# Kernel tuning notes

Hardware: AMD Instinct MI355X
Metric: run time of the kernel (lower is better)

The kernel has to match this reference:

```python
import jax, jax.numpy as jnp
import numpy as np

K = 20  # hard-coded in LPDNet


def act(v):
    # LeakyReLU with negative_slope=0.0 == ReLU
    return jnp.maximum(v, 0.0)


def conv1d(x, w, b):
    # x: (B,C,N), w: (O,C), b: (O,) -> (B,O,N)  (1x1 Conv1d)
    return jnp.einsum('bcn,oc->bon', x, w) + b[None, :, None]


def conv2d(x, w, b):
    # x: (B,C,N,K), w: (O,C), b: (O,) -> (B,O,N,K)  (1x1 Conv2d)
    return jnp.einsum('bcnk,oc->bonk', x, w) + b[None, :, None, None]


def knn(x, k):
    # x: (B,C,N) -> idx (B,N,k) of nearest neighbors by negative squared L2
    xx = jnp.sum(x * x, axis=1)                       # (B,N)
    inner = jnp.einsum('bcn,bcm->bnm', x, x)          # (B,N,N)
    pairwise = 2.0 * inner - xx[:, :, None] - xx[:, None, :]
    _, idx = jax.lax.top_k(pairwise, k)
    return idx


def graph_feature(x, idx):
    # x: (B,C,N), idx: (B,N,k) -> (B,2C,N,k) as concat(neighbor - center, center)
    xt = jnp.transpose(x, (0, 2, 1))                  # (B,N,C)
    nbr = jax.vmap(lambda f, i: f[i])(xt, idx)        # (B,N,k,C)
    ctr = jnp.broadcast_to(xt[:, :, None, :], nbr.shape)
    feat = jnp.concatenate([nbr - ctr, ctr], axis=-1)  # (B,N,k,2C)
    return jnp.transpose(feat, (0, 3, 1, 2))          # (B,2C,N,k)


def setup_inputs():
    key = jax.random.key(0)
    ks = jax.random.split(key, 13)
    p = lambda k, s: jax.random.normal(k, s, jnp.float32) * 0.02
    return {
        'x': jax.random.normal(ks[0], (8, 1, 4096, 3), jnp.float32),
        'w1': p(ks[1], (64, 3)),    'b1': p(ks[2], (64,)),
        'w2': p(ks[3], (64, 64)),   'b2': p(ks[4], (64,)),
        'wdg1': p(ks[5], (128, 128)), 'bdg1': p(ks[6], (128,)),
        'wdg2': p(ks[7], (128, 128)), 'bdg2': p(ks[8], (128,)),
        'wsn1': p(ks[9], (256, 256)), 'bsn1': p(ks[10], (256,)),
        'w3': p(ks[11], (1024, 512)), 'b3': p(ks[12], (1024,)),
    }


def reference(x, w1, b1, w2, b2, wdg1, bdg1, wdg2, bdg2, wsn1, bsn1, w3, b3):
    xp = jnp.transpose(jnp.squeeze(x, 1), (0, 2, 1))  # (B,3,N)
    xinit = xp
    h = act(conv1d(xp, w1, b1))                       # (B,64,N)
    h = act(conv1d(h, w2, b2))                        # (B,64,N)
    idx1 = knn(h, K)
    g = graph_feature(h, idx1)                        # (B,128,N,K)
    g = act(conv2d(g, wdg1, bdg1))                    # (B,128,N,K)
    x1 = jnp.max(g, axis=-1)                          # (B,128,N)
    g = act(conv2d(g, wdg2, bdg2))                    # (B,128,N,K)
    x2 = jnp.max(g, axis=-1)                          # (B,128,N)
    idx2 = knn(xinit, K)                              # knn on raw 3D coords
    g = graph_feature(x2, idx2)                       # (B,256,N,K)
    g = act(conv2d(g, wsn1, bsn1))                    # (B,256,N,K)
    x3 = jnp.max(g, axis=-1)                          # (B,256,N)
    cat = jnp.concatenate([x1, x2, x3], axis=1)       # (B,512,N)
    out = act(conv1d(cat, w3, b3))                    # (B,1024,N)
    return out[..., None]                             # (B,1024,N,1)
```

## Files before the change

kernel.cpp:

```cpp
#include <hip/hip_runtime.h>
#include <stdint.h>


#define NB 8
#define NP 4096
#define NPTS (NB*NP)

typedef float  floatx4 __attribute__((ext_vector_type(4)));
typedef short  short8  __attribute__((ext_vector_type(8)));

__device__ __forceinline__ unsigned short f2bf(float f) {
  union { float f; uint32_t u; } v; v.f = f;
  uint32_t r = v.u + 0x7fffu + ((v.u >> 16) & 1u);
  return (unsigned short)(r >> 16);
}
__device__ __forceinline__ float bf2f(unsigned short h) {
  union { uint32_t u; float f; } v; v.u = ((uint32_t)h) << 16;
  return v.f;
}

__device__ __forceinline__ floatx4 mfma_bf16(short8 a, short8 b, floatx4 c) {
  return __builtin_amdgcn_mfma_f32_16x16x32_bf16(a, b, c, 0, 0, 0);
}

__global__ void cvt_weights(const float* wdg1, unsigned short* wdg1b,
                            const float* wdg2, unsigned short* wdg2b,
                            const float* wsn1, unsigned short* wsn1b,
                            const float* w3, unsigned short* w3b) {
  int i = blockIdx.x * 256 + threadIdx.x;
  if (i < 16384) {
    int c = i & 127;
    wdg1b[i] = f2bf(wdg1[i] - (c >= 64 ? wdg1[i - 64] : 0.f));
  }
  if (i < 16384) wdg2b[i] = f2bf(wdg2[i]);
  if (i < 65536) {
    int c = i & 255;
    wsn1b[i] = f2bf(wsn1[i] - (c >= 128 ? wsn1[i - 128] : 0.f));
  }
  if (i < 524288) w3b[i] = f2bf(w3[i]);
}

__global__ __launch_bounds__(256) void conv12(
    const float* __restrict__ xin, const float* __restrict__ w1,
    const float* __restrict__ b1, const float* __restrict__ w2,
    const float* __restrict__ b2,
    unsigned short* __restrict__ hb16, unsigned short* __restrict__ hlo16,
    float* __restrict__ hh, float* __restrict__ cc) {
  int wave = threadIdx.x >> 6, lane = threadIdx.x & 63;
  int p = blockIdx.x * 4 + wave;
  __shared__ float s_h1[4][64];
  const float* xp = xin + p * 3;
  float c0 = xp[0], c1 = xp[1], c2 = xp[2];
  float v = b1[lane] + w1[lane*3+0]*c0 + w1[lane*3+1]*c1 + w1[lane*3+2]*c2;
  s_h1[wave][lane] = fmaxf(v, 0.f);
  __syncthreads();
  float acc = b2[lane];
  const float* wr = w2 + lane * 64;
  #pragma unroll
  for (int c = 0; c < 64; c += 4) {
    floatx4 w4 = *(const floatx4*)(wr + c);
    acc += w4[0]*s_h1[wave][c]   + w4[1]*s_h1[wave][c+1]
         + w4[2]*s_h1[wave][c+2] + w4[3]*s_h1[wave][c+3];
  }
  acc = fmaxf(acc, 0.f);
  unsigned short hi = f2bf(acc);
  hb16[p*64 + lane] = hi;
  hlo16[p*64 + lane] = f2bf(acc - bf2f(hi));
  float sq = acc * acc;
  #pragma unroll
  for (int off = 32; off; off >>= 1) sq += __shfl_xor(sq, off, 64);
  if (lane == 0) { hh[p] = sq; cc[p] = c0*c0 + c1*c1 + c2*c2; }
}

__global__ __launch_bounds__(256) void knn64_mfma(
    const unsigned short* __restrict__ Hhi, const unsigned short* __restrict__ Hlo,
    const float* __restrict__ XX, int* __restrict__ idx_out) {
  __shared__ unsigned short mhi[128][72];
  __shared__ unsigned short mlo[128][72];
  __shared__ float dots[64][132];
  __shared__ float xxMh[128];
  __shared__ float tau[64];
  int b = blockIdx.y;
  int r0 = blockIdx.x * 64;
  int t = threadIdx.x;
  int lane = t & 63, wave = t >> 6;
  int quad = lane >> 4, l15 = lane & 15;
  const unsigned short* Hhib = Hhi + (size_t)b * NP * 64;
  const unsigned short* Hlob = Hlo + (size_t)b * NP * 64;
  short8 ahi[2], alo[2];
  {
    const unsigned short* pr = Hhib + (size_t)(r0 + wave * 16 + l15) * 64 + quad * 8;
    const unsigned short* pl = Hlob + (size_t)(r0 + wave * 16 + l15) * 64 + quad * 8;
    ahi[0] = *(const short8*)pr; ahi[1] = *(const short8*)(pr + 32);
    alo[0] = *(const short8*)pl; alo[1] = *(const short8*)(pl + 32);
  }
  if (t < 64) tau[t] = -__builtin_inff();

  float lv[20]; int li[20];
  #pragma unroll
  for (int s = 0; s < 20; s++) { lv[s] = -__builtin_inff(); li[s] = 0x7fffffff; }
  float minval = -__builtin_inff(); int minpos = 0;
  int row = t >> 2, sub = t & 3;

  for (int mt = 0; mt < NP / 128; mt++) {
    int m0 = mt * 128;
    {
      int hf = t & 1, r = (t >> 1) & 127;
      int c0 = hf * 32;
      const unsigned short* sh = Hhib + (size_t)(m0 + r) * 64 + c0;
      const unsigned short* sl = Hlob + (size_t)(m0 + r) * 64 + c0;
      *(short8*)&mhi[r][c0]      = *(const short8*)sh;
      *(short8*)&mhi[r][c0 + 8]  = *(const short8*)(sh + 8);
      *(short8*)&mhi[r][c0 + 16] = *(const short8*)(sh + 16);
      *(short8*)&mhi[r][c0 + 24] = *(const short8*)(sh + 24);
      *(short8*)&mlo[r][c0]      = *(const short8*)sl;
      *(short8*)&mlo[r][c0 + 8]  = *(const short8*)(sl + 8);
      *(short8*)&mlo[r][c0 + 16] = *(const short8*)(sl + 16);
      *(short8*)&mlo[r][c0 + 24] = *(const short8*)(sl + 24);
    }
    if (t < 128) xxMh[t] = 0.5f * XX[b * NP + m0 + t];
    __syncthreads();
    #pragma unroll
    for (int nt = 0; nt < 8; nt++) {
      floatx4 acc = (floatx4)0.f;
      #pragma unroll
      for (int ks = 0; ks < 2; ks++) {
        int k0 = ks * 32 + quad * 8;
        short8 bhi = *(short8*)&mhi[nt * 16 + l15][k0];
        short8 blo = *(short8*)&mlo[nt * 16 + l15][k0];
        acc = mfma_bf16(ahi[ks], bhi, acc);
        acc = mfma_bf16(ahi[ks], blo, acc);
        acc = mfma_bf16(alo[ks], bhi, acc);
        acc = mfma_bf16(alo[ks], blo, acc);
      }
      int colg = nt * 16 + l15;
      float xm = xxMh[colg];
      #pragma unroll
      for (int r = 0; r < 4; r++) {
        int mr = wave * 16 + quad * 4 + r;
        dots[mr][colg] = acc[r] - xm;
      }
    }
    __syncthreads();
    float gate = fmaxf(minval, tau[row]);
    floatx4 dv[8];
    #pragma unroll
    for (int q = 0; q < 8; q++) dv[q] = *(floatx4*)&dots[row][sub * 32 + q * 4];
    uint32_t mask = 0;
    #pragma unroll
    for (int q = 0; q < 8; q++)
      #pragma unroll
      for (int j = 0; j < 4; j++)
        if (dv[q][j] > gate) mask |= 1u << (q * 4 + j);
    #pragma clang loop unroll(disable)
    for (int round = 0; round < 32; round++) {
      if (!__any(mask != 0)) break;
      if (mask) {
        int i = __builtin_ctz(mask); mask &= mask - 1;
        float v = dots[row][sub * 32 + i];
        if (v > minval) {
          int gi = m0 + sub * 32 + i;
          #pragma unroll
          for (int s = 0; s < 20; s++)
            if (s == minpos) { lv[s] = v; li[s] = gi; }
          minval = __builtin_inff();
          #pragma unroll
          for (int s = 0; s < 20; s++)
            if (lv[s] < minval) { minval = lv[s]; minpos = s; }
        }
      }
    }
    tau[row] = fmaxf(tau[row], minval);
  }
  int base = (b * NP + r0 + row) * 20;
  for (int sel = 0; sel < 20; sel++) {
    float mybv = -__builtin_inff(); int mybi = 0x7fffffff, mybs = 0;
    #pragma unroll
    for (int s = 0; s < 20; s++) {
      bool better = lv[s] > mybv || (lv[s] == mybv && li[s] < mybi);
      if (better) { mybv = lv[s]; mybi = li[s]; mybs = s; }
    }
    float bv = mybv; int bi = mybi;
    float ov = __shfl_xor(bv, 1, 64); int oi = __shfl_xor(bi, 1, 64);
    if (ov > bv || (ov == bv && oi < bi)) { bv = ov; bi = oi; }
    ov = __shfl_xor(bv, 2, 64); oi = __shfl_xor(bi, 2, 64);
    if (ov > bv || (ov == bv && oi < bi)) { bv = ov; bi = oi; }
    if (sub == 0) idx_out[base + sel] = bi;
    if (bi == mybi) {
      #pragma unroll
      for (int s = 0; s < 20; s++)
        if (s == mybs) { lv[s] = -__builtin_inff(); li[s] = 0x7fffffff; }
    }
  }
}

template<int C>
__global__ __launch_bounds__(256) void knn_topk(
    const float* __restrict__ X, const float* __restrict__ XX,
    int* __restrict__ idx_out) {
  __shared__ float rowsT[C][68];
  __shared__ float mT[C][132];
  __shared__ float dots[64][132];
  __shared__ float xxMh[128];
  __shared__ float tau[64];
  int b = blockIdx.y;
  int r0 = blockIdx.x * 64;
  int t = threadIdx.x;
  const float* Xb = X + (size_t)b * NP * C;
  for (int e = t; e < C * 64; e += 256) {
    int r = e / C, c = e - r * C;
    rowsT[c][r] = Xb[(r0 + r) * C + c];
  }
  if (t < 64) tau[t] = -__builtin_inff();

  float lv[20]; int li[20];
  #pragma unroll
  for (int s = 0; s < 20; s++) { lv[s] = -__builtin_inff(); li[s] = 0x7fffffff; }
  float minval = -__builtin_inff(); int minpos = 0;

  int tm = t & 15, tr = t >> 4;
  int row = t >> 2, sub = t & 3;

  for (int mt = 0; mt < NP / 128; mt++) {
    int m0 = mt * 128;
    for (int e = t; e < C * 128; e += 256) {
      int r = e / C, c = e - r * C;
      mT[c][r] = Xb[(m0 + r) * C + c];
    }
    if (t < 128) xxMh[t] = 0.5f * XX[b * NP + m0 + t];
    __syncthreads();
    float acc[4][8];
    #pragma unroll
    for (int i = 0; i < 4; i++)
      #pragma unroll
      for (int j = 0; j < 8; j++) acc[i][j] = 0.f;
    for (int c = 0; c < C; c++) {
      floatx4 av  = *(floatx4*)&rowsT[c][tr * 4];
      floatx4 bv0 = *(floatx4*)&mT[c][tm * 8];
      floatx4 bv1 = *(floatx4*)&mT[c][tm * 8 + 4];
      #pragma unroll
      for (int i = 0; i < 4; i++)
        #pragma unroll
        for (int j = 0; j < 4; j++) {
          acc[i][j]     += av[i] * bv0[j];
          acc[i][j + 4] += av[i] * bv1[j];
        }
    }
    #pragma unroll
    for (int i = 0; i < 4; i++) {
      floatx4 sv0, sv1;
      #pragma unroll
      for (int j = 0; j < 4; j++) {
        sv0[j] = acc[i][j]     - xxMh[tm*8 + j];
        sv1[j] = acc[i][j + 4] - xxMh[tm*8 + 4 + j];
      }
      *(floatx4*)&dots[tr*4 + i][tm*8]     = sv0;
      *(floatx4*)&dots[tr*4 + i][tm*8 + 4] = sv1;
    }
    __syncthreads();
    float gate = fmaxf(minval, tau[row]);
    floatx4 dv[8];
    #pragma unroll
    for (int q = 0; q < 8; q++) dv[q] = *(floatx4*)&dots[row][sub * 32 + q * 4];
    uint32_t mask = 0;
    #pragma unroll
    for (int q = 0; q < 8; q++)
      #pragma unroll
      for (int j = 0; j < 4; j++)
        if (dv[q][j] > gate) mask |= 1u << (q * 4 + j);
    #pragma clang loop unroll(disable)
    for (int round = 0; round < 32; round++) {
      if (!__any(mask != 0)) break;
      if (mask) {
        int i = __builtin_ctz(mask); mask &= mask - 1;
        float v = dots[row][sub * 32 + i];
        if (v > minval) {
          int gi = m0 + sub * 32 + i;
          #pragma unroll
          for (int s = 0; s < 20; s++)
            if (s == minpos) { lv[s] = v; li[s] = gi; }
          minval = __builtin_inff();
          #pragma unroll
          for (int s = 0; s < 20; s++)
            if (lv[s] < minval) { minval = lv[s]; minpos = s; }
        }
      }
    }
    tau[row] = fmaxf(tau[row], minval);
  }
  int base = (b * NP + r0 + row) * 20;
  for (int sel = 0; sel < 20; sel++) {
    float mybv = -__builtin_inff(); int mybi = 0x7fffffff, mybs = 0;
    #pragma unroll
    for (int s = 0; s < 20; s++) {
      bool better = lv[s] > mybv || (lv[s] == mybv && li[s] < mybi);
      if (better) { mybv = lv[s]; mybi = li[s]; mybs = s; }
    }
    float bv = mybv; int bi = mybi;
    float ov = __shfl_xor(bv, 1, 64); int oi = __shfl_xor(bi, 1, 64);
    if (ov > bv || (ov == bv && oi < bi)) { bv = ov; bi = oi; }
    ov = __shfl_xor(bv, 2, 64); oi = __shfl_xor(bi, 2, 64);
    if (ov > bv || (ov == bv && oi < bi)) { bv = ov; bi = oi; }
    if (sub == 0) idx_out[base + sel] = bi;
    if (bi == mybi) {
      #pragma unroll
      for (int s = 0; s < 20; s++)
        if (s == mybs) { lv[s] = -__builtin_inff(); li[s] = 0x7fffffff; }
    }
  }
}

__global__ __launch_bounds__(256) void dg_stage(
    const unsigned short* __restrict__ hb16, const int* __restrict__ idx1,
    const unsigned short* __restrict__ w1b, const float* __restrict__ bia1,
    const unsigned short* __restrict__ w2b, const float* __restrict__ bia2,
    unsigned short* __restrict__ featb) {
  __shared__ unsigned short s_a[80][136];
  __shared__ unsigned short s_v[80][136];
  __shared__ int s_nbf[80];
  int p0 = blockIdx.x * 4;
  int b = p0 >> 12, n0 = p0 & 4095;
  int t = threadIdx.x;
  int lane = t & 63, wave = t >> 6;
  if (t < 80) s_nbf[t] = idx1[p0 * 20 + t];
  __syncthreads();
  const unsigned short* hbb = hb16 + (size_t)b * NP * 64;
  {
    int cc = (t & 15) * 8;
    int r00 = t >> 4;
    #pragma unroll
    for (int it = 0; it < 5; it++) {
      int row = r00 + it * 16;
      const unsigned short* src = (cc < 64)
        ? hbb + (size_t)s_nbf[row] * 64 + cc
        : hbb + (size_t)(n0 + row / 20) * 64 + (cc - 64);
      *(short8*)&s_a[row][cc] = *(const short8*)src;
    }
  }
  __syncthreads();
  int quad = lane >> 4, mrow = lane & 15;
  int nblock = wave * 32;
  {
    floatx4 acc[5][2];
    #pragma unroll
    for (int mt = 0; mt < 5; mt++) { acc[mt][0] = (floatx4)0.f; acc[mt][1] = (floatx4)0.f; }
    #pragma unroll
    for (int ks = 0; ks < 4; ks++) {
      int k0 = ks * 32 + quad * 8;
      short8 w0 = *(const short8*)(w1b + (nblock + mrow) * 128 + k0);
      short8 w1v = *(const short8*)(w1b + (nblock + 16 + mrow) * 128 + k0);
      #pragma unroll
      for (int mt = 0; mt < 5; mt++) {
        short8 a = *(short8*)&s_a[mt * 16 + mrow][k0];
        acc[mt][0] = mfma_bf16(a, w0, acc[mt][0]);
        acc[mt][1] = mfma_bf16(a, w1v, acc[mt][1]);
      }
    }
    #pragma unroll
    for (int ns = 0; ns < 2; ns++) {
      int o = nblock + ns * 16 + mrow;
      float bz = bia1[o];
      #pragma unroll
      for (int mt = 0; mt < 5; mt++)
        #pragma unroll
        for (int r = 0; r < 4; r++)
          s_v[mt * 16 + quad * 4 + r][o] = f2bf(fmaxf(acc[mt][ns][r] + bz, 0.f));
    }
  }
  __syncthreads();
  #pragma unroll
  for (int it = 0; it < 2; it++) {
    int e = t + it * 256;
    int pt = e >> 7, o = e & 127;
    float mx = 0.f;
    for (int k = 0; k < 20; k++) mx = fmaxf(mx, bf2f(s_v[pt * 20 + k][o]));
    featb[(size_t)(p0 + pt) * 512 + o] = f2bf(mx);
  }
  {
    floatx4 acc[5][2];
    #pragma unroll
    for (int mt = 0; mt < 5; mt++) { acc[mt][0] = (floatx4)0.f; acc[mt][1] = (floatx4)0.f; }
    #pragma unroll
    for (int ks = 0; ks < 4; ks++) {
      int k0 = ks * 32 + quad * 8;
      short8 w0 = *(const short8*)(w2b + (nblock + mrow) * 128 + k0);
      short8 w1v = *(const short8*)(w2b + (nblock + 16 + mrow) * 128 + k0);
      #pragma unroll
      for (int mt = 0; mt < 5; mt++) {
        short8 a = *(short8*)&s_v[mt * 16 + mrow][k0];
        acc[mt][0] = mfma_bf16(a, w0, acc[mt][0]);
        acc[mt][1] = mfma_bf16(a, w1v, acc[mt][1]);
      }
    }
    #pragma unroll
    for (int ns = 0; ns < 2; ns++) {
      int o = nblock + ns * 16 + mrow;
      float bz = bia2[o];
      #pragma unroll
      for (int mt = 0; mt < 5; mt++)
        #pragma unroll
        for (int r = 0; r < 4; r++)
          s_a[mt * 16 + quad * 4 + r][o] = f2bf(fmaxf(acc[mt][ns][r] + bz, 0.f));
    }
  }
  __syncthreads();
  #pragma unroll
  for (int it = 0; it < 2; it++) {
    int e = t + it * 256;
    int pt = e >> 7, o = e & 127;
    float mx = 0.f;
    for (int k = 0; k < 20; k++) mx = fmaxf(mx, bf2f(s_a[pt * 20 + k][o]));
    featb[(size_t)(p0 + pt) * 512 + 128 + o] = f2bf(mx);
  }
}

__global__ __launch_bounds__(256) void sn_stage(
    const int* __restrict__ idx2, const unsigned short* __restrict__ wb,
    const float* __restrict__ bias, unsigned short* __restrict__ featb) {
  __shared__ unsigned short s_a[80][264];
  __shared__ int s_nbf[80];
  int p0 = blockIdx.x * 4;
  int b = p0 >> 12, n0 = p0 & 4095;
  int bb = b << 12;
  int t = threadIdx.x;
  int lane = t & 63, wave = t >> 6;
  if (t < 80) s_nbf[t] = idx2[p0 * 20 + t];
  __syncthreads();
  {
    int cc = (t & 31) * 8;
    int r00 = t >> 5;
    #pragma unroll
    for (int it = 0; it < 10; it++) {
      int row = r00 + it * 8;
      const unsigned short* src = (cc < 128)
        ? featb + (size_t)(bb + s_nbf[row]) * 512 + 128 + cc
        : featb + (size_t)(bb + n0 + row / 20) * 512 + cc;
      *(short8*)&s_a[row][cc] = *(const short8*)src;
    }
  }
  __syncthreads();
  int quad = lane >> 4, mrow = lane & 15;
  int nblock = wave * 64;
  floatx4 acc[5][4];
  #pragma unroll
  for (int mt = 0; mt < 5; mt++)
    #pragma unroll
    for (int ns = 0; ns < 4; ns++) acc[mt][ns] = (floatx4)0.f;
  #pragma unroll
  for (int ks = 0; ks < 8; ks++) {
    int k0 = ks * 32 + quad * 8;
    short8 w[4];
    #pragma unroll
    for (int ns = 0; ns < 4; ns++)
      w[ns] = *(const short8*)(wb + (nblock + ns * 16 + mrow) * 256 + k0);
    #pragma unroll
    for (int mt = 0; mt < 5; mt++) {
      short8 a = *(short8*)&s_a[mt * 16 + mrow][k0];
      #pragma unroll
      for (int ns = 0; ns < 4; ns++)
        acc[mt][ns] = mfma_bf16(a, w[ns], acc[mt][ns]);
    }
  }
  __syncthreads();
  #pragma unroll
  for (int ns = 0; ns < 4; ns++) {
    int o = nblock + ns * 16 + mrow;
    float bz = bias[o];
    #pragma unroll
    for (int mt = 0; mt < 5; mt++)
      #pragma unroll
      for (int r = 0; r < 4; r++)
        s_a[mt * 16 + quad * 4 + r][o] = f2bf(fmaxf(acc[mt][ns][r] + bz, 0.f));
  }
  __syncthreads();
  #pragma unroll
  for (int it = 0; it < 4; it++) {
    int e = t + it * 256;
    int pt = e >> 8, o = e & 255;
    float mx = 0.f;
    for (int k = 0; k < 20; k++) mx = fmaxf(mx, bf2f(s_a[pt * 20 + k][o]));
    featb[(size_t)(p0 + pt) * 512 + 256 + o] = f2bf(mx);
  }
}

__global__ __launch_bounds__(256) void conv3_gemm(
    const unsigned short* __restrict__ w3b, const unsigned short* __restrict__ featb,
    const float* __restrict__ b3, float* __restrict__ out) {
  __shared__ unsigned short s_a[128][40];
  __shared__ unsigned short s_b[128][40];
  int o0 = blockIdx.x * 128, p0 = blockIdx.y * 128;
  int t = threadIdx.x, lane = t & 63, wave = t >> 6;
  int wy = wave >> 1, wx = wave & 1;
  int quad = lane >> 4, l15 = lane & 15;
  floatx4 acc[4][4];
  #pragma unroll
  for (int i = 0; i < 4; i++)
    #pragma unroll
    for (int j = 0; j < 4; j++) acc[i][j] = (floatx4)0.f;
  for (int kc = 0; kc < 16; kc++) {
    __syncthreads();
    for (int e = t; e < 512; e += 256) {
      int r = e >> 2, c8 = (e & 3) * 8;
      *(short8*)&s_a[r][c8] = *(const short8*)(w3b + (size_t)(o0 + r) * 512 + kc * 32 + c8);
    }
    for (int e = t; e < 512; e += 256) {
      int r = e >> 2, c8 = (e & 3) * 8;
      *(short8*)&s_b[r][c8] = *(const short8*)(featb + (size_t)(p0 + r) * 512 + kc * 32 + c8);
    }
    __syncthreads();
    int k0 = quad * 8;
    short8 af[4], bfr[4];
    #pragma unroll
    for (int i = 0; i < 4; i++) af[i] = *(short8*)&s_a[wy * 64 + i * 16 + l15][k0];
    #pragma unroll
    for (int j = 0; j < 4; j++) bfr[j] = *(short8*)&s_b[wx * 64 + j * 16 + l15][k0];
    #pragma unroll
    for (int i = 0; i < 4; i++)
      #pragma unroll
      for (int j = 0; j < 4; j++) acc[i][j] = mfma_bf16(af[i], bfr[j], acc[i][j]);
  }
  #pragma unroll
  for (int i = 0; i < 4; i++)
    #pragma unroll
    for (int j = 0; j < 4; j++) {
      int pl = p0 + wx * 64 + j * 16 + l15;
      int bI = pl >> 12, n = pl & 4095;
      #pragma unroll
      for (int r = 0; r < 4; r++) {
        int o = o0 + wy * 64 + i * 16 + quad * 4 + r;
        out[(size_t)(bI * 1024 + o) * 4096 + n] = fmaxf(acc[i][j][r] + b3[o], 0.f);
      }
    }
}

extern "C" void kernel_launch(void* const* d_in, const int* in_sizes, int n_in,
                              void* d_out, int out_size, void* d_ws, size_t ws_size,
                              hipStream_t stream) {
  const float* x    = (const float*)d_in[0];
  const float* w1   = (const float*)d_in[1];
  const float* b1   = (const float*)d_in[2];
  const float* w2   = (const float*)d_in[3];
  const float* b2   = (const float*)d_in[4];
  const float* wdg1 = (const float*)d_in[5];
  const float* bdg1 = (const float*)d_in[6];
  const float* wdg2 = (const float*)d_in[7];
  const float* bdg2 = (const float*)d_in[8];
  const float* wsn1 = (const float*)d_in[9];
  const float* bsn1 = (const float*)d_in[10];
  const float* w3   = (const float*)d_in[11];
  const float* b3   = (const float*)d_in[12];

  float* ws = (float*)d_ws;
  unsigned short* hlo16 = (unsigned short*)ws;
  float* hh = ws + 2097152;
  float* cc = ws + 2129920;
  int* idx1 = (int*)(ws + 2162688);
  int* idx2 = (int*)(ws + 2818048);
  unsigned short* featb = (unsigned short*)(ws + 3473408);
  unsigned short* wdg1b = (unsigned short*)(ws + 11862016);
  unsigned short* wdg2b = (unsigned short*)(ws + 11870208);
  unsigned short* wsn1b = (unsigned short*)(ws + 11878400);
  unsigned short* w3b   = (unsigned short*)(ws + 11911168);
  unsigned short* hb16  = (unsigned short*)(ws + 12173312);

  cvt_weights<<<2048, 256, 0, stream>>>(wdg1, wdg1b, wdg2, wdg2b,
                                        wsn1, wsn1b, w3, w3b);
  conv12<<<8192, 256, 0, stream>>>(x, w1, b1, w2, b2, hb16, hlo16, hh, cc);
  knn64_mfma<<<dim3(64, 8), 256, 0, stream>>>(hb16, hlo16, hh, idx1);
  knn_topk<3><<<dim3(64, 8), 256, 0, stream>>>(x, cc, idx2);
  dg_stage<<<8192, 256, 0, stream>>>(hb16, idx1, wdg1b, bdg1, wdg2b, bdg2, featb);
  sn_stage<<<8192, 256, 0, stream>>>(idx2, wsn1b, bsn1, featb);
  conv3_gemm<<<dim3(8, 256), 256, 0, stream>>>(w3b, featb, b3, (float*)d_out);
}
```

Measured before the change: 991.5 us.

## Fuse the two KNN kernels into one launch with interleaved block flavors

```diff
diff --git a/kernel.cpp b/kernel.cpp
--- a/kernel.cpp
+++ b/kernel.cpp
@@ -72,16 +72,18 @@
   if (lane == 0) { hh[p] = sq; cc[p] = c0*c0 + c1*c1 + c2*c2; }
 }
 
-__global__ __launch_bounds__(256) void knn64_mfma(
+
+__device__ __forceinline__ void knn64_body(
+    unsigned char* smem,
     const unsigned short* __restrict__ Hhi, const unsigned short* __restrict__ Hlo,
-    const float* __restrict__ XX, int* __restrict__ idx_out) {
-  __shared__ unsigned short mhi[128][72];
-  __shared__ unsigned short mlo[128][72];
-  __shared__ float dots[64][132];
-  __shared__ float xxMh[128];
-  __shared__ float tau[64];
-  int b = blockIdx.y;
-  int r0 = blockIdx.x * 64;
+    const float* __restrict__ XX, int* __restrict__ idx_out,
+    int xt, int b) {
+  auto mhi  = (unsigned short (*)[72])(smem);
+  auto mlo  = (unsigned short (*)[72])(smem + 18432);
+  auto dots = (float (*)[132])(smem + 36864);
+  float* xxMh = (float*)(smem + 70656);
+  float* tau  = (float*)(smem + 71168);
+  int r0 = xt * 64;
   int t = threadIdx.x;
   int lane = t & 63, wave = t >> 6;
   int quad = lane >> 4, l15 = lane & 15;
@@ -194,17 +196,17 @@
   }
 }
 
-template<int C>
-__global__ __launch_bounds__(256) void knn_topk(
+__device__ __forceinline__ void knn3_body(
+    unsigned char* smem,
     const float* __restrict__ X, const float* __restrict__ XX,
-    int* __restrict__ idx_out) {
-  __shared__ float rowsT[C][68];
-  __shared__ float mT[C][132];
-  __shared__ float dots[64][132];
-  __shared__ float xxMh[128];
-  __shared__ float tau[64];
-  int b = blockIdx.y;
-  int r0 = blockIdx.x * 64;
+    int* __restrict__ idx_out, int xt, int b) {
+  constexpr int C = 3;
+  auto rowsT = (float (*)[68])(smem);
+  auto mT    = (float (*)[132])(smem + 816);
+  auto dots  = (float (*)[132])(smem + 2400);
+  float* xxMh = (float*)(smem + 36192);
+  float* tau  = (float*)(smem + 36704);
+  int r0 = xt * 64;
   int t = threadIdx.x;
   const float* Xb = X + (size_t)b * NP * C;
   for (int e = t; e < C * 64; e += 256) {
@@ -310,6 +312,22 @@
   }
 }
 
+__global__ __launch_bounds__(256) void knn_fused(
+    const unsigned short* __restrict__ Hhi, const unsigned short* __restrict__ Hlo,
+    const float* __restrict__ HH,
+    const float* __restrict__ X, const float* __restrict__ CC,
+    int* __restrict__ idx1, int* __restrict__ idx2) {
+  __shared__ __attribute__((aligned(16))) unsigned char smem[71424];
+  int id = blockIdx.x;
+  int flavor = (id >> 8) & 1;
+  int slot = (id & 255) | ((id >> 9) << 8);
+  int b = slot >> 6, xt = slot & 63;
+  if (flavor == 0)
+    knn64_body(smem, Hhi, Hlo, HH, idx1, xt, b);
+  else
+    knn3_body(smem, X, CC, idx2, xt, b);
+}
+
 __global__ __launch_bounds__(256) void dg_stage(
     const unsigned short* __restrict__ hb16, const int* __restrict__ idx1,
     const unsigned short* __restrict__ w1b, const float* __restrict__ bia1,
@@ -566,8 +584,7 @@
   cvt_weights<<<2048, 256, 0, stream>>>(wdg1, wdg1b, wdg2, wdg2b,
                                         wsn1, wsn1b, w3, w3b);
   conv12<<<8192, 256, 0, stream>>>(x, w1, b1, w2, b2, hb16, hlo16, hh, cc);
-  knn64_mfma<<<dim3(64, 8), 256, 0, stream>>>(hb16, hlo16, hh, idx1);
-  knn_topk<3><<<dim3(64, 8), 256, 0, stream>>>(x, cc, idx2);
+  knn_fused<<<1024, 256, 0, stream>>>(hb16, hlo16, hh, x, cc, idx1, idx2);
   dg_stage<<<8192, 256, 0, stream>>>(hb16, idx1, wdg1b, bdg1, wdg2b, bdg2, featb);
   sn_stage<<<8192, 256, 0, stream>>>(idx2, wsn1b, bsn1, featb);
   conv3_gemm<<<dim3(8, 256), 256, 0, stream>>>(w3b, featb, b3, (float*)d_out);
```

New measurement: 969.7 us. -2.2%, faster.

## Merge 3D kNN top-k and DG stage into one heterogeneous launch

Applied to the files above, without the earlier changes.

```diff
diff --git a/kernel.cpp b/kernel.cpp
--- a/kernel.cpp
+++ b/kernel.cpp
@@ -194,17 +194,18 @@
   }
 }
 
-template<int C>
-__global__ __launch_bounds__(256) void knn_topk(
+
+__device__ __forceinline__ void knn3_body(
+    unsigned char* smem,
     const float* __restrict__ X, const float* __restrict__ XX,
-    int* __restrict__ idx_out) {
-  __shared__ float rowsT[C][68];
-  __shared__ float mT[C][132];
-  __shared__ float dots[64][132];
-  __shared__ float xxMh[128];
-  __shared__ float tau[64];
-  int b = blockIdx.y;
-  int r0 = blockIdx.x * 64;
+    int* __restrict__ idx_out, int xt, int b) {
+  constexpr int C = 3;
+  auto rowsT = (float (*)[68])(smem);
+  auto mT    = (float (*)[132])(smem + 816);
+  auto dots  = (float (*)[132])(smem + 2400);
+  float* xxMh = (float*)(smem + 36192);
+  float* tau  = (float*)(smem + 36704);
+  int r0 = xt * 64;
   int t = threadIdx.x;
   const float* Xb = X + (size_t)b * NP * C;
   for (int e = t; e < C * 64; e += 256) {
@@ -310,15 +311,16 @@
   }
 }
 
-__global__ __launch_bounds__(256) void dg_stage(
+__device__ __forceinline__ void dg_body(
+    unsigned char* smem,
     const unsigned short* __restrict__ hb16, const int* __restrict__ idx1,
     const unsigned short* __restrict__ w1b, const float* __restrict__ bia1,
     const unsigned short* __restrict__ w2b, const float* __restrict__ bia2,
-    unsigned short* __restrict__ featb) {
-  __shared__ unsigned short s_a[80][136];
-  __shared__ unsigned short s_v[80][136];
-  __shared__ int s_nbf[80];
-  int p0 = blockIdx.x * 4;
+    unsigned short* __restrict__ featb, int pid) {
+  auto s_a = (unsigned short (*)[136])(smem);
+  auto s_v = (unsigned short (*)[136])(smem + 21760);
+  int* s_nbf = (int*)(smem + 43520);
+  int p0 = pid * 4;
   int b = p0 >> 12, n0 = p0 & 4095;
   int t = threadIdx.x;
   int lane = t & 63, wave = t >> 6;
@@ -412,6 +414,21 @@
     for (int k = 0; k < 20; k++) mx = fmaxf(mx, bf2f(s_a[pt * 20 + k][o]));
     featb[(size_t)(p0 + pt) * 512 + 128 + o] = f2bf(mx);
   }
+}
+
+__global__ __launch_bounds__(256) void knn3_dg(
+    const float* __restrict__ X, const float* __restrict__ CC,
+    int* __restrict__ idx2,
+    const unsigned short* __restrict__ hb16, const int* __restrict__ idx1,
+    const unsigned short* __restrict__ w1b, const float* __restrict__ bia1,
+    const unsigned short* __restrict__ w2b, const float* __restrict__ bia2,
+    unsigned short* __restrict__ featb) {
+  __shared__ __attribute__((aligned(16))) unsigned char smem[43840];
+  int id = blockIdx.x;
+  if (id < 512)
+    knn3_body(smem, X, CC, idx2, id & 63, id >> 6);
+  else
+    dg_body(smem, hb16, idx1, w1b, bia1, w2b, bia2, featb, id - 512);
 }
 
 __global__ __launch_bounds__(256) void sn_stage(
@@ -567,8 +584,8 @@
                                         wsn1, wsn1b, w3, w3b);
   conv12<<<8192, 256, 0, stream>>>(x, w1, b1, w2, b2, hb16, hlo16, hh, cc);
   knn64_mfma<<<dim3(64, 8), 256, 0, stream>>>(hb16, hlo16, hh, idx1);
-  knn_topk<3><<<dim3(64, 8), 256, 0, stream>>>(x, cc, idx2);
-  dg_stage<<<8192, 256, 0, stream>>>(hb16, idx1, wdg1b, bdg1, wdg2b, bdg2, featb);
+  knn3_dg<<<8704, 256, 0, stream>>>(x, cc, idx2, hb16, idx1,
+                                    wdg1b, bdg1, wdg2b, bdg2, featb);
   sn_stage<<<8192, 256, 0, stream>>>(idx2, wsn1b, bsn1, featb);
   conv3_gemm<<<dim3(8, 256), 256, 0, stream>>>(w3b, featb, b3, (float*)d_out);
 }
```

Result: no change. 992.3 us (+0.1%).
